# Kernel optimization log

Measured on AMD Instinct MI355X. Metric: run time of the kernel, lower is better.

## Reference

```python
import jax, jax.numpy as jnp
import numpy as np

B, S, H, I, E, TOP_K = 1, 2048, 1024, 4096, 8, 1


def setup_inputs() -> dict:
    key = jax.random.key(0)
    ks = jax.random.split(key, 8)
    s = 0.02  # init scale for weights
    return {
        "hidden_states": jax.random.normal(ks[0], (B, S, H), jnp.float32),
        "router_w": jax.random.normal(ks[1], (E, H), jnp.float32) * s,
        "w_gate": jax.random.normal(ks[2], (E, I, H), jnp.float32) * s,
        "w_up": jax.random.normal(ks[3], (E, I, H), jnp.float32) * s,
        "w_down": jax.random.normal(ks[4], (E, H, I), jnp.float32) * s,
        "ws_gate": jax.random.normal(ks[5], (I, H), jnp.float32) * s,
        "ws_up": jax.random.normal(ks[6], (I, H), jnp.float32) * s,
        "ws_down": jax.random.normal(ks[7], (H, I), jnp.float32) * s,
    }


def _mlp(x, wg, wu, wd):
    # silu(x @ Wg^T) * (x @ Wu^T) @ Wd^T  (Llama4TextMLP)
    return (jax.nn.silu(x @ wg.T) * (x @ wu.T)) @ wd.T


def reference(hidden_states, router_w, w_gate, w_up, w_down, ws_gate, ws_up, ws_down):
    b, s, h = hidden_states.shape
    hs = hidden_states.reshape(-1, h)                      # [T, H]
    T = hs.shape[0]
    logits = hs @ router_w.T                               # [T, E]
    top_v, top_i = jax.lax.top_k(logits, TOP_K)            # [T, K]
    masked = jnp.full_like(logits, -jnp.inf)
    masked = masked.at[jnp.arange(T)[:, None], top_i].set(top_v)
    scores = jax.nn.sigmoid(masked)                        # [T, E]; sigmoid(-inf)=0

    # In this module every expert sees ALL tokens, scaled by its (mostly-zero) score.
    routed = scores.T[:, :, None] * hs[None, :, :]         # [E, T, H]

    out = _mlp(hs, ws_gate, ws_up, ws_down)                # shared expert, [T, H]
    gate = jnp.einsum('eth,eih->eti', routed, w_gate)      # [E, T, I]
    up = jnp.einsum('eth,eih->eti', routed, w_up)          # [E, T, I]
    expert_out = jnp.einsum('eti,ehi->eth', jax.nn.silu(gate) * up, w_down)
    out = out + expert_out.sum(axis=0)                     # [T, H]
    return out, scores.T                                   # router_scores is [E, T]
```

## Files before the change

kernel.cpp:

```cpp
#include <hip/hip_runtime.h>
#include <hip/hip_bf16.h>
#include <math.h>

#define T_TOK 2048
#define HDIM 1024
#define IDIM 4096
#define NEXP 8
#define RROWS 3200
#define AROWS 5248
#define ZROW  5120
#define NP2   24
#define BK 32

typedef unsigned int uint;
typedef unsigned short ushort;
typedef __attribute__((ext_vector_type(4))) float f32x4;
typedef __attribute__((ext_vector_type(8))) short bf16x8;

__device__ __forceinline__ ushort f2bf(float f) {
  union { float f; uint u; } c; c.f = f;
  uint u = c.u;
  return (ushort)((u + 0x7FFFu + ((u >> 16) & 1u)) >> 16);
}
__device__ __forceinline__ uint cvtpk(float a, float b) {
  uint r;
  asm("v_cvt_pk_bf16_f32 %0, %1, %2" : "=v"(r) : "v"(a), "v"(b));
  return r;
}
__device__ __forceinline__ uint4 cvt8(const float4 a, const float4 b) {
  uint4 r;
  r.x = cvtpk(a.x, a.y); r.y = cvtpk(a.z, a.w);
  r.z = cvtpk(b.x, b.y); r.w = cvtpk(b.z, b.w);
  return r;
}
__device__ __forceinline__ void gld16(ushort* lds, const ushort* g) {
  __builtin_amdgcn_global_load_lds(
      (const __attribute__((address_space(1))) uint*)g,
      (__attribute__((address_space(3))) uint*)lds, 16, 0, 0);
}
__device__ __forceinline__ int soff(int row, int kc) {
  return ((row >> 4) << 9) + (kc << 7) + ((row & 15) << 3);
}

#define SYNCV(N) { \
  __builtin_amdgcn_sched_barrier(0); \
  asm volatile("s_waitcnt vmcnt(" #N ") lgkmcnt(0)" ::: "memory"); \
  __builtin_amdgcn_s_barrier(); \
  __builtin_amdgcn_sched_barrier(0); }

__global__ __launch_bounds__(256) void router_kernel(
    const float* __restrict__ hs, const float* __restrict__ rw,
    ushort* __restrict__ Xall, float* __restrict__ scores_out,
    int* __restrict__ eidx, float* __restrict__ sval)
{
  const int wave = threadIdx.x >> 6;
  const int lane = threadIdx.x & 63;
  const int t = blockIdx.x * 4 + wave;
  const float* row = hs + (size_t)t * HDIM;
  float v[16];
  #pragma unroll
  for (int i = 0; i < 16; ++i) {
    v[i] = row[lane + 64 * i];
    Xall[(size_t)t * HDIM + lane + 64 * i] = f2bf(v[i]);
  }
  float logit[8];
  #pragma unroll
  for (int e = 0; e < 8; ++e) {
    const float* wr = rw + e * HDIM;
    float s = 0.f;
    #pragma unroll
    for (int i = 0; i < 16; ++i) s += v[i] * wr[lane + 64 * i];
    #pragma unroll
    for (int off = 32; off; off >>= 1) s += __shfl_xor(s, off, 64);
    logit[e] = s;
  }
  if (lane == 0) {
    int be = 0; float bv = logit[0];
    #pragma unroll
    for (int e = 1; e < 8; ++e) if (logit[e] > bv) { bv = logit[e]; be = e; }
    float sc = 1.f / (1.f + expf(-bv));
    eidx[t] = be; sval[t] = sc;
    #pragma unroll
    for (int e = 0; e < 8; ++e) scores_out[(size_t)e * T_TOK + t] = (e == be) ? sc : 0.f;
  }
}

__global__ __launch_bounds__(256) void plan_kernel(
    const int* __restrict__ eidx, int* __restrict__ row2tok, int4* __restrict__ pairs)
{
  __shared__ int cnt[8];
  __shared__ int slot[8];
  const int tid = threadIdx.x;
  if (tid < 8) cnt[tid] = 0;
  __syncthreads();
  for (int t = tid; t < T_TOK; t += 256) atomicAdd(&cnt[eidx[t]], 1);
  __syncthreads();
  if (tid == 0) {
    int np = 0;
    for (int i = 0; i < 8; ++i) pairs[np++] = make_int4(i * 256, i * 256 + 128, -1, 1);
    int o = 0;
    for (int e = 0; e < 8; ++e) {
      slot[e] = o;
      int cap = (cnt[e] + 127) & ~127;
      int nt = cap / 128;
      for (int j = 0; j < nt; j += 2) {
        int ra = T_TOK + o + j * 128;
        int rb = (j + 1 < nt) ? ra + 128 : ZROW;
        pairs[np++] = make_int4(ra, rb, e, 1);
      }
      o += cap;
    }
    for (; np < NP2; ++np) pairs[np] = make_int4(ZROW, ZROW, 0, 0);
  }
  for (int r = tid; r < RROWS; r += 256) row2tok[r] = -1;
  __syncthreads();
  for (int t = tid; t < T_TOK; t += 256) {
    int e = eidx[t];
    int s = atomicAdd(&slot[e], 1);
    row2tok[s] = t;
  }
}

__global__ __launch_bounds__(256) void gather_kernel(
    const float* __restrict__ hs, const int* __restrict__ row2tok,
    const float* __restrict__ sval, ushort* __restrict__ Xall)
{
  const int r = blockIdx.x;
  const int t = row2tok[r];
  const int c0 = threadIdx.x * 4;
  ushort4 o;
  if (t >= 0) {
    const float sc = sval[t];
    float4 v = *(const float4*)(hs + (size_t)t * HDIM + c0);
    o.x = f2bf(sc * v.x); o.y = f2bf(sc * v.y); o.z = f2bf(sc * v.z); o.w = f2bf(sc * v.w);
  } else { o.x = o.y = o.z = o.w = 0; }
  *(ushort4*)(Xall + (size_t)(T_TOK + r) * HDIM + c0) = o;
}

#define LOADB1(S, k0) { \
  gr##S = *(const float4*)(gptr + (k0)); \
  ur##S = *(const float4*)(uptr + (k0)); }

#define WRITEB1(S, B) { \
  *(uint2*)&Bg[B][woff] = make_uint2(cvtpk(gr##S.x, gr##S.y), cvtpk(gr##S.z, gr##S.w)); \
  *(uint2*)&Bu[B][woff] = make_uint2(cvtpk(ur##S.x, ur##S.y), cvtpk(ur##S.z, ur##S.w)); }

#define STAGEA1(ABASE, k0) { gld16((ABASE) + alds0, asrc0 + (k0)); }

#define READ1(ABASE, B) \
  bf16x8 af[4], gf[2], uf[2]; \
  _Pragma("unroll") \
  for (int m = 0; m < 4; ++m) af[m] = *(const bf16x8*)((ABASE) + (wm*4+m)*512 + lp); \
  _Pragma("unroll") \
  for (int n = 0; n < 2; ++n) { \
    gf[n] = *(const bf16x8*)&Bg[B][(wn*2+n)*512 + lp]; \
    uf[n] = *(const bf16x8*)&Bu[B][(wn*2+n)*512 + lp]; }

#define MFMA1 \
  _Pragma("unroll") \
  for (int m = 0; m < 4; ++m) { \
    _Pragma("unroll") \
    for (int n = 0; n < 2; ++n) { \
      accg[m][n] = __builtin_amdgcn_mfma_f32_16x16x32_bf16(af[m], gf[n], accg[m][n], 0, 0, 0); \
      accu[m][n] = __builtin_amdgcn_mfma_f32_16x16x32_bf16(af[m], uf[n], accu[m][n], 0, 0, 0); } }

#define ROTA { ushort* aT_ = aR; aR = aM; aM = aS; aS = aT_; }

__global__ __launch_bounds__(1024, 1) void gemm1_kernel(
    const ushort* __restrict__ Xall,
    const float* __restrict__ w_gate, const float* __restrict__ w_up,
    const float* __restrict__ ws_gate, const float* __restrict__ ws_up,
    const int4* __restrict__ pairs, ushort* __restrict__ actall)
{
  __shared__ __align__(16) ushort As[3][8192];
  __shared__ __align__(16) ushort Bg[2][4096];
  __shared__ __align__(16) ushort Bu[2][4096];

  const int b0 = blockIdx.x;
  const int j = b0 & 7, s = b0 >> 3;
  const int panel = j + 8 * (s / NP2);
  const int4 td = pairs[s % NP2];
  if (td.w == 0) return;
  const int r0a = td.x, r0b = td.y, e = td.z;
  const float* __restrict__ gbase = (e < 0) ? ws_gate : w_gate + (size_t)e * IDIM * HDIM;
  const float* __restrict__ ubase = (e < 0) ? ws_up   : w_up   + (size_t)e * IDIM * HDIM;
  const int col0 = panel * 128;

  const int tid = threadIdx.x;
  const int lane = tid & 63;
  const int w = tid >> 6;
  const int wm = w >> 2, wn = w & 3;

  const int brow = tid >> 3, bch = tid & 7;
  const float* gptr = gbase + (size_t)(col0 + brow) * HDIM + bch * 4;
  const float* uptr = ubase + (size_t)(col0 + brow) * HDIM + bch * 4;
  const int woff = soff(brow, bch >> 1) + (bch & 1) * 4;

  const size_t abs0 = (w < 8) ? (size_t)(r0a + w * 16 + (lane & 15))
                              : (size_t)(r0b + (w - 8) * 16 + (lane & 15));
  const ushort* asrc0 = Xall + abs0 * HDIM + (lane >> 4) * 8;
  const int alds0 = w * 512 + lane * 8;

  ushort* aR = &As[0][0];
  ushort* aM = &As[1][0];
  ushort* aS = &As[2][0];

  float4 gr0, ur0, gr1, ur1;
  const int lp = (lane >> 4) * 128 + (lane & 15) * 8;
  f32x4 accg[4][2] = {};
  f32x4 accu[4][2] = {};

  STAGEA1(aR, 0);
  LOADB1(0, 0);
  STAGEA1(aM, BK);
  LOADB1(1, BK);
  WRITEB1(0, 0);
  SYNCV(3);

  const int NS = HDIM / BK;
  for (int kk = 0; kk < NS / 2 - 1; ++kk) {
    const int k = kk * 2;
    {
      READ1(aR, 0);
      STAGEA1(aS, (k + 2) * BK);
      LOADB1(0, (k + 2) * BK);
      MFMA1;
      WRITEB1(1, 1);
      SYNCV(3);
      ROTA;
    }
    {
      READ1(aR, 1);
      STAGEA1(aS, (k + 3) * BK);
      LOADB1(1, (k + 3) * BK);
      MFMA1;
      WRITEB1(0, 0);
      SYNCV(3);
      ROTA;
    }
  }
  {
    READ1(aR, 0);
    MFMA1;
    WRITEB1(1, 1);
    SYNCV(0);
    ROTA;
  }
  {
    READ1(aR, 1);
    MFMA1;
  }

  const int prbase = wm * 64 + ((lane >> 4) << 2);
  const int cbase = col0 + wn * 32 + (lane & 15);
  #pragma unroll
  for (int m = 0; m < 4; ++m)
    #pragma unroll
    for (int n = 0; n < 2; ++n)
      #pragma unroll
      for (int j2 = 0; j2 < 4; ++j2) {
        const int pr = prbase + m * 16 + j2;
        const size_t ar = (wm < 2) ? (size_t)(r0a + pr) : (size_t)(r0b + pr - 128);
        float g = accg[m][n][j2];
        float u = accu[m][n][j2];
        float sv = g / (1.f + __expf(-g)) * u;
        actall[ar * IDIM + cbase + n * 16] = f2bf(sv);
      }
}

#define LOADB2(S, k0) { \
  const float4* bp_ = (const float4*)(bptr + (k0)); \
  br##S[0] = bp_[0]; br##S[1] = bp_[1]; }

#define WRITEB2(S, B) { *(uint4*)&Bs[B][woff2] = cvt8(br##S[0], br##S[1]); }

#define STAGEA2(B, k0) { \
  gld16(&As[B][alds0], asrc0 + (k0)); \
  gld16(&As[B][alds1], asrc1 + (k0)); }

#define READ2(B) \
  bf16x8 af[4], bfr[4]; \
  _Pragma("unroll") \
  for (int m = 0; m < 4; ++m) af[m] = *(const bf16x8*)&As[B][(wm*4+m)*512 + lp]; \
  _Pragma("unroll") \
  for (int n = 0; n < 4; ++n) bfr[n] = *(const bf16x8*)&Bs[B][(wn*4+n)*512 + lp];

#define MFMA2 \
  _Pragma("unroll") \
  for (int m = 0; m < 4; ++m) { \
    _Pragma("unroll") \
    for (int n = 0; n < 4; ++n) \
      acc[m][n] = __builtin_amdgcn_mfma_f32_16x16x32_bf16(af[m], bfr[n], acc[m][n], 0, 0, 0); }

__global__ __launch_bounds__(512, 1) void gemm2_kernel(
    const ushort* __restrict__ actall,
    const float* __restrict__ w_down, const float* __restrict__ ws_down,
    const int4* __restrict__ pairs, const int* __restrict__ row2tok,
    float* __restrict__ out, float* __restrict__ bufr)
{
  __shared__ __align__(16) ushort As[2][8192];
  __shared__ __align__(16) ushort Bs[2][4096];

  const int b0 = blockIdx.x;
  const int panel = b0 & 7;
  const int4 td = pairs[b0 >> 3];
  if (td.w == 0) return;
  const int r0a = td.x, r0b = td.y, e = td.z;
  const float* __restrict__ bbase = (e < 0) ? ws_down : w_down + (size_t)e * HDIM * IDIM;
  const int col0 = panel * 128;

  const int tid = threadIdx.x;
  const int lane = tid & 63;
  const int w = tid >> 6;
  const int wm = w >> 1, wn = w & 1;

  const int brow = tid >> 2, kcb = tid & 3;
  const float* bptr = bbase + (size_t)(col0 + brow) * IDIM + kcb * 8;
  const int woff2 = soff(brow, kcb);

  const int arow = w * 32 + (lane & 15);
  const size_t abs0 = (w < 4) ? (size_t)(r0a + arow) : (size_t)(r0b + arow - 128);
  const ushort* asrc0 = actall + abs0 * IDIM + (lane >> 4) * 8;
  const ushort* asrc1 = asrc0 + (size_t)16 * IDIM;
  const int alds0 = w * 1024 + lane * 8;
  const int alds1 = alds0 + 512;

  float4 br0[2], br1[2];
  const int lp = (lane >> 4) * 128 + (lane & 15) * 8;
  f32x4 acc[4][4] = {};

  STAGEA2(0, 0);
  __builtin_amdgcn_sched_barrier(0);
  LOADB2(0, 0);
  WRITEB2(0, 0);
  LOADB2(1, BK);
  SYNCV(2);

  const int NS = IDIM / BK;
  for (int kk = 0; kk < NS / 2 - 1; ++kk) {
    const int k = kk * 2;
    {
      READ2(0);
      STAGEA2(1, (k + 1) * BK);
      __builtin_amdgcn_sched_barrier(0);
      WRITEB2(1, 1);
      LOADB2(0, (k + 2) * BK);
      MFMA2;
      SYNCV(2);
    }
    {
      READ2(1);
      STAGEA2(0, (k + 2) * BK);
      __builtin_amdgcn_sched_barrier(0);
      WRITEB2(0, 0);
      LOADB2(1, (k + 3) * BK);
      MFMA2;
      SYNCV(2);
    }
  }
  {
    READ2(0);
    STAGEA2(1, (NS - 1) * BK);
    __builtin_amdgcn_sched_barrier(0);
    WRITEB2(1, 1);
    MFMA2;
    SYNCV(0);
  }
  {
    READ2(1);
    MFMA2;
  }

  const int prbase = wm * 64 + ((lane >> 4) << 2);
  const int cbase = col0 + wn * 64 + (lane & 15);
  #pragma unroll
  for (int m = 0; m < 4; ++m)
    #pragma unroll
    for (int j2 = 0; j2 < 4; ++j2) {
      const int pr = prbase + m * 16 + j2;
      const int ar = (wm < 2) ? (r0a + pr) : (r0b + pr - 128);
      if (e < 0) {
        #pragma unroll
        for (int n = 0; n < 4; ++n)
          out[(size_t)ar * HDIM + cbase + n * 16] = acc[m][n][j2];
      } else {
        const int t = row2tok[ar - T_TOK];
        if (t >= 0) {
          #pragma unroll
          for (int n = 0; n < 4; ++n)
            bufr[(size_t)t * HDIM + cbase + n * 16] = acc[m][n][j2];
        }
      }
    }
}

__global__ __launch_bounds__(256) void add_kernel(
    float* __restrict__ out, const float* __restrict__ bufr)
{
  const size_t i = ((size_t)blockIdx.x * 256 + threadIdx.x) * 4;
  float4 a = *(float4*)(out + i);
  const float4 b = *(const float4*)(bufr + i);
  a.x += b.x; a.y += b.y; a.z += b.z; a.w += b.w;
  *(float4*)(out + i) = a;
}

extern "C" void kernel_launch(void* const* d_in, const int* in_sizes, int n_in,
                              void* d_out, int out_size, void* d_ws, size_t ws_size,
                              hipStream_t stream)
{
  const float* hs      = (const float*)d_in[0];
  const float* rw      = (const float*)d_in[1];
  const float* w_gate  = (const float*)d_in[2];
  const float* w_up    = (const float*)d_in[3];
  const float* w_down  = (const float*)d_in[4];
  const float* ws_gate = (const float*)d_in[5];
  const float* ws_up   = (const float*)d_in[6];
  const float* ws_down = (const float*)d_in[7];

  float* out = (float*)d_out;
  float* scores_out = out + (size_t)T_TOK * HDIM;

  char* ws = (char*)d_ws;
  ushort* Xall   = (ushort*)ws;
  ushort* actall = (ushort*)(ws + 10747904);
  float*  bufr   = (float*)(ws + 53739520);
  int*    eidx   = (int*)(ws + 62128128);
  float*  sval   = (float*)(ws + 62136320);
  int*    r2t    = (int*)(ws + 62144512);
  int4*   pairs  = (int4*)(ws + 62157312);

  router_kernel<<<T_TOK / 4, 256, 0, stream>>>(hs, rw, Xall, scores_out, eidx, sval);
  plan_kernel<<<1, 256, 0, stream>>>(eidx, r2t, pairs);
  gather_kernel<<<RROWS, 256, 0, stream>>>(hs, r2t, sval, Xall);
  gemm1_kernel<<<(IDIM / 128) * NP2, 1024, 0, stream>>>(
      Xall, w_gate, w_up, ws_gate, ws_up, pairs, actall);
  gemm2_kernel<<<(HDIM / 128) * NP2, 512, 0, stream>>>(
      actall, w_down, ws_down, pairs, r2t, out, bufr);
  add_kernel<<<(T_TOK * HDIM) / 1024, 256, 0, stream>>>(out, bufr);
}
```

Baseline: 295.8 us.

## Stream fp32 weights straight to LDS asynchronously with a 3-stage pipeline

In gemm1, the gate and up weight tiles are now copied as fp32 directly from global memory into LDS with global_load_lds, using an XOR-swizzled layout. They are no longer loaded into registers, converted to bf16 and stored to LDS. Weight tiles now share the three-buffer rotation the activation tiles use, so the separate register write step and its extra barrier disappear. In exchange, each wave converts fp32 to bf16 when it reads a fragment, which repeats the conversion across the wave rows. LDS traffic and footprint also double, to about 144KB, which may add bank pressure.

```diff
diff --git a/kernel.cpp b/kernel.cpp
--- a/kernel.cpp
+++ b/kernel.cpp
@@ -34,6 +34,11 @@
   return r;
 }
 __device__ __forceinline__ void gld16(ushort* lds, const ushort* g) {
+  __builtin_amdgcn_global_load_lds(
+      (const __attribute__((address_space(1))) uint*)g,
+      (__attribute__((address_space(3))) uint*)lds, 16, 0, 0);
+}
+__device__ __forceinline__ void gld16f(float* lds, const float* g) {
   __builtin_amdgcn_global_load_lds(
       (const __attribute__((address_space(1))) uint*)g,
       (__attribute__((address_space(3))) uint*)lds, 16, 0, 0);
@@ -137,24 +142,26 @@
   *(ushort4*)(Xall + (size_t)(T_TOK + r) * HDIM + c0) = o;
 }
 
-#define LOADB1(S, k0) { \
-  gr##S = *(const float4*)(gptr + (k0)); \
-  ur##S = *(const float4*)(uptr + (k0)); }
-
-#define WRITEB1(S, B) { \
-  *(uint2*)&Bg[B][woff] = make_uint2(cvtpk(gr##S.x, gr##S.y), cvtpk(gr##S.z, gr##S.w)); \
-  *(uint2*)&Bu[B][woff] = make_uint2(cvtpk(ur##S.x, ur##S.y), cvtpk(ur##S.z, ur##S.w)); }
-
-#define STAGEA1(ABASE, k0) { gld16((ABASE) + alds0, asrc0 + (k0)); }
-
-#define READ1(ABASE, B) \
+#define STAGE1(AP, GP, UP, k0) { \
+  gld16((AP) + alds0, asrc0 + (k0)); \
+  gld16f((GP) + blds0, gsrc + (k0)); \
+  gld16f((UP) + blds0, usrc + (k0)); }
+
+#define BFRAG(DST, BASE, N) { \
+  const float* bp_ = (BASE) + (wn * 32 + (N) * 16 + (lane & 15)) * 32; \
+  float4 lo_ = *(const float4*)(bp_ + dlo4); \
+  float4 hi_ = *(const float4*)(bp_ + dhi4); \
+  uint4 uu_; \
+  uu_.x = cvtpk(lo_.x, lo_.y); uu_.y = cvtpk(lo_.z, lo_.w); \
+  uu_.z = cvtpk(hi_.x, hi_.y); uu_.w = cvtpk(hi_.z, hi_.w); \
+  DST = *(bf16x8*)&uu_; }
+
+#define READ1X(AP, GP, UP) \
   bf16x8 af[4], gf[2], uf[2]; \
   _Pragma("unroll") \
-  for (int m = 0; m < 4; ++m) af[m] = *(const bf16x8*)((ABASE) + (wm*4+m)*512 + lp); \
-  _Pragma("unroll") \
-  for (int n = 0; n < 2; ++n) { \
-    gf[n] = *(const bf16x8*)&Bg[B][(wn*2+n)*512 + lp]; \
-    uf[n] = *(const bf16x8*)&Bu[B][(wn*2+n)*512 + lp]; }
+  for (int m = 0; m < 4; ++m) af[m] = *(const bf16x8*)((AP) + (wm*4+m)*512 + lp); \
+  _Pragma("unroll") \
+  for (int n = 0; n < 2; ++n) { BFRAG(gf[n], GP, n); BFRAG(uf[n], UP, n); }
 
 #define MFMA1 \
   _Pragma("unroll") \
@@ -164,7 +171,10 @@
       accg[m][n] = __builtin_amdgcn_mfma_f32_16x16x32_bf16(af[m], gf[n], accg[m][n], 0, 0, 0); \
       accu[m][n] = __builtin_amdgcn_mfma_f32_16x16x32_bf16(af[m], uf[n], accu[m][n], 0, 0, 0); } }
 
-#define ROTA { ushort* aT_ = aR; aR = aM; aM = aS; aS = aT_; }
+#define ROT3 { \
+  ushort* at_ = aR; aR = aM; aM = aS; aS = at_; \
+  float* bt_ = bgR; bgR = bgM; bgM = bgS; bgS = bt_; \
+  bt_ = buR; buR = buM; buM = buS; buS = bt_; }
 
 __global__ __launch_bounds__(1024, 1) void gemm1_kernel(
     const ushort* __restrict__ Xall,
@@ -173,13 +183,13 @@
     const int4* __restrict__ pairs, ushort* __restrict__ actall)
 {
   __shared__ __align__(16) ushort As[3][8192];
-  __shared__ __align__(16) ushort Bg[2][4096];
-  __shared__ __align__(16) ushort Bu[2][4096];
+  __shared__ __align__(16) float  Bg[3][4096];
+  __shared__ __align__(16) float  Bu[3][4096];
 
   const int b0 = blockIdx.x;
-  const int j = b0 & 7, s = b0 >> 3;
-  const int panel = j + 8 * (s / NP2);
-  const int4 td = pairs[s % NP2];
+  const int j = b0 & 7, s0 = b0 >> 3;
+  const int panel = j + 8 * (s0 / NP2);
+  const int4 td = pairs[s0 % NP2];
   if (td.w == 0) return;
   const int r0a = td.x, r0b = td.y, e = td.z;
   const float* __restrict__ gbase = (e < 0) ? ws_gate : w_gate + (size_t)e * IDIM * HDIM;
@@ -191,63 +201,48 @@
   const int w = tid >> 6;
   const int wm = w >> 2, wn = w & 3;
 
-  const int brow = tid >> 3, bch = tid & 7;
-  const float* gptr = gbase + (size_t)(col0 + brow) * HDIM + bch * 4;
-  const float* uptr = ubase + (size_t)(col0 + brow) * HDIM + bch * 4;
-  const int woff = soff(brow, bch >> 1) + (bch & 1) * 4;
+  const int brow = tid >> 3;
+  const int bchg = (tid & 7) ^ (brow & 7);
+  const float* gsrc = gbase + (size_t)(col0 + brow) * HDIM + bchg * 4;
+  const float* usrc = ubase + (size_t)(col0 + brow) * HDIM + bchg * 4;
+  const int blds0 = tid * 4;
 
   const size_t abs0 = (w < 8) ? (size_t)(r0a + w * 16 + (lane & 15))
                               : (size_t)(r0b + (w - 8) * 16 + (lane & 15));
   const ushort* asrc0 = Xall + abs0 * HDIM + (lane >> 4) * 8;
   const int alds0 = w * 512 + lane * 8;
 
-  ushort* aR = &As[0][0];
-  ushort* aM = &As[1][0];
-  ushort* aS = &As[2][0];
-
-  float4 gr0, ur0, gr1, ur1;
+  ushort* aR = &As[0][0]; ushort* aM = &As[1][0]; ushort* aS = &As[2][0];
+  float* bgR = &Bg[0][0]; float* bgM = &Bg[1][0]; float* bgS = &Bg[2][0];
+  float* buR = &Bu[0][0]; float* buM = &Bu[1][0]; float* buS = &Bu[2][0];
+
   const int lp = (lane >> 4) * 128 + (lane & 15) * 8;
+  const int dlo = (((lane >> 4) << 1)) ^ (lane & 7);
+  const int dlo4 = dlo * 4;
+  const int dhi4 = (dlo ^ 1) * 4;
   f32x4 accg[4][2] = {};
   f32x4 accu[4][2] = {};
 
-  STAGEA1(aR, 0);
-  LOADB1(0, 0);
-  STAGEA1(aM, BK);
-  LOADB1(1, BK);
-  WRITEB1(0, 0);
+  STAGE1(aR, bgR, buR, 0);
+  STAGE1(aM, bgM, buM, BK);
   SYNCV(3);
 
   const int NS = HDIM / BK;
-  for (int kk = 0; kk < NS / 2 - 1; ++kk) {
-    const int k = kk * 2;
-    {
-      READ1(aR, 0);
-      STAGEA1(aS, (k + 2) * BK);
-      LOADB1(0, (k + 2) * BK);
-      MFMA1;
-      WRITEB1(1, 1);
-      SYNCV(3);
-      ROTA;
-    }
-    {
-      READ1(aR, 1);
-      STAGEA1(aS, (k + 3) * BK);
-      LOADB1(1, (k + 3) * BK);
-      MFMA1;
-      WRITEB1(0, 0);
-      SYNCV(3);
-      ROTA;
-    }
+  for (int s = 0; s < NS - 2; ++s) {
+    STAGE1(aS, bgS, buS, (s + 2) * BK);
+    READ1X(aR, bgR, buR);
+    MFMA1;
+    SYNCV(3);
+    ROT3;
   }
   {
-    READ1(aR, 0);
+    READ1X(aR, bgR, buR);
     MFMA1;
-    WRITEB1(1, 1);
     SYNCV(0);
-    ROTA;
+    ROT3;
   }
   {
-    READ1(aR, 1);
+    READ1X(aR, bgR, buR);
     MFMA1;
   }
 
```

New measurement: 350.2 us. +18.4%, slower.
